# Optimization experiments

Measured on AMD Instinct MI355X. Metric: run time of the kernel, lower is better.

The kernel has to match this reference:

```python
import jax, jax.numpy as jnp
import numpy as np

N, E, F_IN, H, D = 50000, 800000, 128, 4, 32
NEG_SLOPE = 0.2

def setup_inputs() -> dict:
    key = jax.random.key(0)
    ks = jax.random.split(key, 8)
    x = jax.random.normal(ks[0], (N, F_IN), dtype=jnp.float32)
    src = jax.random.randint(ks[1], (E,), 0, N, dtype=jnp.int32)
    dst = jax.random.randint(ks[2], (E,), 0, N, dtype=jnp.int32)
    s = 1.0 / np.sqrt(F_IN)
    W_src = jax.random.uniform(ks[3], (F_IN, H * D), jnp.float32, -s, s)
    b_src = jnp.zeros((H * D,), jnp.float32)
    W_dst = jax.random.uniform(ks[4], (F_IN, H * D), jnp.float32, -s, s)
    b_dst = jnp.zeros((H * D,), jnp.float32)
    attn = jax.random.normal(ks[5], (H, D), dtype=jnp.float32) / np.sqrt(D)
    return {"x": x, "src": src, "dst": dst, "W_src": W_src, "b_src": b_src,
            "W_dst": W_dst, "b_dst": b_dst, "attn": attn}

def reference(x, src, dst, W_src, b_src, W_dst, b_dst, attn):
    n = x.shape[0]
    # dense projections: [N, H, D]
    fs = (x @ W_src + b_src).reshape(n, H, D)
    fd = (x @ W_dst + b_dst).reshape(n, H, D)
    # GATv2 edge score: a^T leaky_relu(W_l x_u + W_r x_v)
    e = jax.nn.leaky_relu(fs[src] + fd[dst], NEG_SLOPE)  # [E, H, D]
    score = jnp.einsum('ehd,hd->eh', e, attn)            # [E, H]
    # segment softmax over incoming edges of each dst node
    smax = jax.ops.segment_max(score, dst, num_segments=n)
    smax = jnp.where(jnp.isfinite(smax), smax, 0.0)
    ex = jnp.exp(score - smax[dst])
    denom = jax.ops.segment_sum(ex, dst, num_segments=n)
    alpha = ex / denom[dst]                              # [E, H]
    # scatter-weighted aggregation of src features
    h = jax.ops.segment_sum(alpha[:, :, None] * fs[src], dst, num_segments=n)
    h = jax.nn.relu(h)                                   # activation=relu
    return h.reshape(n, H * D)
```

## Files before the change

kernel.cpp:

```cpp
#include <hip/hip_runtime.h>
#include <hip/hip_fp16.h>

#define NN 50000
#define NE 800000
#define FIN 128
#define NH 4
#define HD 32
#define FOUT 128
#define NEG 0.2f
#define NB_W    ((256 * FIN + 255) / 256)
#define N_GEMM  782
#define NBKT    98
#define CHUNK   4096
#define NCHUNK  ((NE + CHUNK - 1) / CHUNK)
#define GB_GRID 980
#define BCAP    12288

typedef __attribute__((ext_vector_type(8))) short bf16x8;
typedef __attribute__((ext_vector_type(4))) float f32x4;

__device__ __forceinline__ uint f2bf_u(float f) {
    uint u = __float_as_uint(f);
    u += 0x7FFF + ((u >> 16) & 1);
    return u >> 16;
}
__device__ __forceinline__ ushort f2bf(float f) { return (ushort)f2bf_u(f); }

template<int CTRL>
__device__ __forceinline__ float dpp_add(float x) {
    int y = __builtin_amdgcn_update_dpp(0, __float_as_int(x), CTRL, 0xF, 0xF, false);
    return x + __int_as_float(y);
}
#define DPP_QUAD_XOR1 0xB1
#define DPP_QUAD_XOR2 0x4E

__device__ __forceinline__ __half2 u2h(uint u) { return __builtin_bit_cast(__half2, u); }
__device__ __forceinline__ uint h2u(__half2 h) { return __builtin_bit_cast(uint, h); }

__device__ __forceinline__ __half2 hmax2(__half2 a, __half2 b) {
    uint r, ua = h2u(a), ub = h2u(b);
    asm("v_pk_max_f16 %0, %1, %2" : "=v"(r) : "v"(ua), "v"(ub));
    return u2h(r);
}

__global__ __launch_bounds__(256) void hist_wt_k(
    const int* __restrict__ dst, int* __restrict__ chunk_hist,
    const float* __restrict__ Wsrc, const float* __restrict__ Wdst,
    ushort* __restrict__ Wt,
    const float* __restrict__ attn, __half* __restrict__ attn_h)
{
    __shared__ int hist[NBKT];
    const int b = blockIdx.x;
    const int tid = threadIdx.x;
    if (b < NCHUNK) {
        const int e0 = b * CHUNK;
        for (int t = tid; t < NBKT; t += 256) hist[t] = 0;
        __syncthreads();
        #pragma unroll
        for (int k = 0; k < 16; ++k) {
            const int e = e0 + k * 256 + tid;
            if (e < NE) atomicAdd(&hist[dst[e] >> 9], 1);
        }
        __syncthreads();
        for (int t = tid; t < NBKT; t += 256)
            chunk_hist[b * NBKT + t] = hist[t];
    } else {
        if (b == NCHUNK && tid < FOUT) attn_h[tid] = __float2half(attn[tid]);
        int t = (b - NCHUNK) * 256 + tid;
        if (t >= 256 * FIN) return;
        int n = t >> 7, k = t & 127;
        float v = (n < 128) ? Wsrc[k * 128 + n] : Wdst[k * 128 + (n - 128)];
        Wt[t] = f2bf(v);
    }
}

__global__ __launch_bounds__(256) void gemm_scatter_k(
    const float* __restrict__ x, const ushort* __restrict__ Wt,
    const float* __restrict__ bsrc, const float* __restrict__ bdst,
    __half* __restrict__ fsfd,
    const int* __restrict__ dst, const int* __restrict__ src,
    const int* __restrict__ chunk_hist, int* __restrict__ bkbase,
    uint* __restrict__ ebuf)
{
    __shared__ ushort As[64 * 128];
    __shared__ ushort Bs[64 * 128];
    __shared__ int cur[NBKT];
    __shared__ int tot_s[NBKT];
    __shared__ int par_s[NBKT];
    __shared__ int ps[256];
    const int b = blockIdx.x;
    const int tid = threadIdx.x;

    if (b % 5 == 0) {
        const int chunk = b / 5;
        for (int t = tid; t < NBKT; t += 256) { tot_s[t] = 0; par_s[t] = 0; }
        __syncthreads();
        #pragma unroll 4
        for (int i = tid; i < NCHUNK * NBKT; i += 256) {
            const int v = chunk_hist[i];
            const int c = i / NBKT;
            const int t = i - c * NBKT;
            atomicAdd(&tot_s[t], v);
            if (c < chunk) atomicAdd(&par_s[t], v);
        }
        __syncthreads();
        const int total = (tid < NBKT) ? tot_s[tid] : 0;
        ps[tid] = total;
        __syncthreads();
        for (int off = 1; off < 256; off <<= 1) {
            int add = (tid >= off) ? ps[tid - off] : 0;
            __syncthreads();
            ps[tid] += add;
            __syncthreads();
        }
        if (tid < NBKT) cur[tid] = (ps[tid] - total) + par_s[tid];
        if (chunk == 0) {
            if (tid < NBKT) bkbase[tid] = ps[tid] - total;
            if (tid == 0) bkbase[NBKT] = NE;
        }
        __syncthreads();
        const int e0 = chunk * CHUNK;
        #pragma unroll
        for (int k = 0; k < 16; ++k) {
            const int e = e0 + k * 256 + tid;
            if (e < NE) {
                const int d = dst[e];
                const int p = atomicAdd(&cur[d >> 9], 1);
                ebuf[p] = ((uint)d << 16) | (uint)src[e];
            }
        }
        return;
    }

    const int g = b - b / 5 - 1;
    if (g >= N_GEMM) return;
    const int bm = g * 64;

    for (int q = tid; q < 64 * 16; q += 256) {
        int r = q >> 4, c16 = q & 15;
        int row = bm + r;
        uint4 o = make_uint4(0u, 0u, 0u, 0u);
        if (row < NN) {
            const float4 a = *(const float4*)&x[(size_t)row * FIN + c16 * 8];
            const float4 c = *(const float4*)&x[(size_t)row * FIN + c16 * 8 + 4];
            o.x = f2bf_u(a.x) | (f2bf_u(a.y) << 16);
            o.y = f2bf_u(a.z) | (f2bf_u(a.w) << 16);
            o.z = f2bf_u(c.x) | (f2bf_u(c.y) << 16);
            o.w = f2bf_u(c.z) | (f2bf_u(c.w) << 16);
        }
        int off = r * 256 + ((c16 * 16) ^ ((r & 7) << 4));
        *(uint4*)((char*)As + off) = o;
    }

    const int wid = tid >> 6, lane = tid & 63;
    const int wr = (wid >> 1) * 32, wc = (wid & 1) * 32;
    const int lrow = lane & 15;
    const int lk = (lane >> 4) * 16;

    #pragma unroll
    for (int ct = 0; ct < 4; ++ct) {
        if (ct > 0) __syncthreads();
        for (int q = tid; q < 64 * 16; q += 256) {
            int r = q >> 4, c16 = q & 15;
            uint4 v = *(const uint4*)&Wt[(ct * 64 + r) * FIN + c16 * 8];
            int off = r * 256 + ((c16 * 16) ^ ((r & 7) << 4));
            *(uint4*)((char*)Bs + off) = v;
        }
        __syncthreads();

        f32x4 acc[2][2] = {};
        #pragma unroll
        for (int kk = 0; kk < 4; ++kk) {
            bf16x8 a[2], bb[2];
            #pragma unroll
            for (int m = 0; m < 2; ++m) {
                int r = wr + m * 16 + lrow;
                int off = r * 256 + ((kk * 64 + lk) ^ ((r & 7) << 4));
                a[m] = *(bf16x8*)((char*)As + off);
            }
            #pragma unroll
            for (int n = 0; n < 2; ++n) {
                int r = wc + n * 16 + lrow;
                int off = r * 256 + ((kk * 64 + lk) ^ ((r & 7) << 4));
                bb[n] = *(bf16x8*)((char*)Bs + off);
            }
            #pragma unroll
            for (int m = 0; m < 2; ++m)
                #pragma unroll
                for (int n = 0; n < 2; ++n)
                    acc[m][n] = __builtin_amdgcn_mfma_f32_16x16x32_bf16(a[m], bb[n], acc[m][n], 0, 0, 0);
        }

        #pragma unroll
        for (int m = 0; m < 2; ++m) {
            #pragma unroll
            for (int n = 0; n < 2; ++n) {
                int gcol = ct * 64 + wc + n * 16 + (lane & 15);
                float bias = (gcol < 128) ? bsrc[gcol] : bdst[gcol - 128];
                #pragma unroll
                for (int r = 0; r < 4; ++r) {
                    int grow = bm + wr + m * 16 + (lane >> 4) * 4 + r;
                    if (grow < NN)
                        fsfd[(size_t)grow * 256 + gcol] = __float2half(acc[m][n][r] + bias);
                }
            }
        }
    }
}

__global__ __launch_bounds__(256) void binB_k(
    const uint* __restrict__ ebuf, const int* __restrict__ bkbase,
    int* __restrict__ rowptr, ushort* __restrict__ nbr)
{
    __shared__ int cnt_s[512];
    __shared__ int ps[256];
    __shared__ ushort buf[BCAP];
    const int b = blockIdx.x;
    const int tid = threadIdx.x;
    const int node0 = b << 9;
    const int nodes = (node0 + 512 < NN) ? 512 : (NN - node0);
    const int segbase = bkbase[b];
    const int segend  = bkbase[b + 1];
    const int seglen  = segend - segbase;

    cnt_s[tid] = 0;
    cnt_s[tid + 256] = 0;
    __syncthreads();
    for (int i = segbase + tid; i < segend; i += 256)
        atomicAdd(&cnt_s[(int)(ebuf[i] >> 16) - node0], 1);
    __syncthreads();

    const int c0 = cnt_s[2 * tid], c1 = cnt_s[2 * tid + 1];
    const int pair = c0 + c1;
    ps[tid] = pair;
    __syncthreads();
    for (int off = 1; off < 256; off <<= 1) {
        int add = (tid >= off) ? ps[tid - off] : 0;
        __syncthreads();
        ps[tid] += add;
        __syncthreads();
    }
    const int ex = ps[tid] - pair;
    __syncthreads();
    cnt_s[2 * tid] = ex;
    cnt_s[2 * tid + 1] = ex + c0;
    if (2 * tid < nodes)     rowptr[node0 + 2 * tid]     = segbase + ex;
    if (2 * tid + 1 < nodes) rowptr[node0 + 2 * tid + 1] = segbase + ex + c0;
    if (b == NBKT - 1 && tid == 0) rowptr[NN] = segend;
    __syncthreads();

    if (seglen <= BCAP) {
        for (int i = segbase + tid; i < segend; i += 256) {
            const uint e = ebuf[i];
            const int d = (int)(e >> 16) - node0;
            const int p = atomicAdd(&cnt_s[d], 1);
            buf[p] = (ushort)(e & 0xffffu);
        }
        __syncthreads();
        for (int i = tid; i < seglen; i += 256)
            nbr[segbase + i] = buf[i];
    } else {
        for (int i = segbase + tid; i < segend; i += 256) {
            const uint e = ebuf[i];
            const int d = (int)(e >> 16) - node0;
            const int p = atomicAdd(&cnt_s[d], 1);
            nbr[segbase + p] = (ushort)(e & 0xffffu);
        }
    }
}

__global__ __launch_bounds__(256) void gat_node_k(
    const __half* __restrict__ fsfd, const __half* __restrict__ attn_h,
    const int* __restrict__ rowptr, const ushort* __restrict__ nbr,
    float* __restrict__ out)
{
    const int node = blockIdx.x * 4 + (threadIdx.x >> 6);
    const int lane = threadIdx.x & 63;
    const int ql = lane & 15;
    const int q  = lane >> 4;

    const uint4 ufd = *(const uint4*)&fsfd[(size_t)node * 256 + 128 + 8 * ql];
    const __half2 fd0 = u2h(ufd.x), fd1 = u2h(ufd.y), fd2 = u2h(ufd.z), fd3 = u2h(ufd.w);
    const uint4 uav = *(const uint4*)&attn_h[8 * ql];
    const __half2 av0 = u2h(uav.x), av1 = u2h(uav.y), av2 = u2h(uav.z), av3 = u2h(uav.w);
    const __half2 k02 = __float2half2_rn(NEG);

    const int beg = rowptr[node];
    const int end = rowptr[node + 1];

    float den = 0.f;
    __half2 acc0 = u2h(0), acc1 = u2h(0), acc2 = u2h(0), acc3 = u2h(0);

    for (int i = beg; i < end; i += 16) {
        #pragma unroll
        for (int j = 0; j < 4; ++j) {
            const int idx = i + 4 * j + q;
            const bool valid = idx < end;
            const int s = nbr[valid ? idx : end - 1];
            const uint4 u = *(const uint4*)&fsfd[(size_t)s * 256 + 8 * ql];
            const __half2 f0 = u2h(u.x), f1 = u2h(u.y), f2 = u2h(u.z), f3 = u2h(u.w);
            __half2 v0 = __hadd2(f0, fd0), v1 = __hadd2(f1, fd1);
            __half2 v2 = __hadd2(f2, fd2), v3 = __hadd2(f3, fd3);
            v0 = hmax2(v0, __hmul2(v0, k02));
            v1 = hmax2(v1, __hmul2(v1, k02));
            v2 = hmax2(v2, __hmul2(v2, k02));
            v3 = hmax2(v3, __hmul2(v3, k02));
            __half2 sch = __hmul2(v0, av0);
            sch = __hfma2(v1, av1, sch);
            sch = __hfma2(v2, av2, sch);
            sch = __hfma2(v3, av3, sch);
            float sc = __low2float(sch) + __high2float(sch);
            sc = dpp_add<DPP_QUAD_XOR1>(sc);
            sc = dpp_add<DPP_QUAD_XOR2>(sc);
            float ex = __expf(sc);
            ex = valid ? ex : 0.f;
            den += ex;
            const __half2 exh = __float2half2_rn(ex);
            acc0 = __hfma2(exh, f0, acc0);
            acc1 = __hfma2(exh, f1, acc1);
            acc2 = __hfma2(exh, f2, acc2);
            acc3 = __hfma2(exh, f3, acc3);
        }
    }

    den += __shfl_xor(den, 16, 64);
    den += __shfl_xor(den, 32, 64);
    uint ua0 = h2u(acc0), ua1 = h2u(acc1), ua2 = h2u(acc2), ua3 = h2u(acc3);
    ua0 = h2u(__hadd2(u2h(ua0), u2h((uint)__shfl_xor((int)ua0, 16, 64))));
    ua1 = h2u(__hadd2(u2h(ua1), u2h((uint)__shfl_xor((int)ua1, 16, 64))));
    ua2 = h2u(__hadd2(u2h(ua2), u2h((uint)__shfl_xor((int)ua2, 16, 64))));
    ua3 = h2u(__hadd2(u2h(ua3), u2h((uint)__shfl_xor((int)ua3, 16, 64))));
    ua0 = h2u(__hadd2(u2h(ua0), u2h((uint)__shfl_xor((int)ua0, 32, 64))));
    ua1 = h2u(__hadd2(u2h(ua1), u2h((uint)__shfl_xor((int)ua1, 32, 64))));
    ua2 = h2u(__hadd2(u2h(ua2), u2h((uint)__shfl_xor((int)ua2, 32, 64))));
    ua3 = h2u(__hadd2(u2h(ua3), u2h((uint)__shfl_xor((int)ua3, 32, 64))));

    if (q == 0) {
        const float inv = (den > 0.f) ? 1.f / den : 0.f;
        float4 o0, o1;
        o0.x = fmaxf(__low2float(u2h(ua0))  * inv, 0.f);
        o0.y = fmaxf(__high2float(u2h(ua0)) * inv, 0.f);
        o0.z = fmaxf(__low2float(u2h(ua1))  * inv, 0.f);
        o0.w = fmaxf(__high2float(u2h(ua1)) * inv, 0.f);
        o1.x = fmaxf(__low2float(u2h(ua2))  * inv, 0.f);
        o1.y = fmaxf(__high2float(u2h(ua2)) * inv, 0.f);
        o1.z = fmaxf(__low2float(u2h(ua3))  * inv, 0.f);
        o1.w = fmaxf(__high2float(u2h(ua3)) * inv, 0.f);
        *(float4*)&out[(size_t)node * FOUT + 8 * ql] = o0;
        *(float4*)&out[(size_t)node * FOUT + 8 * ql + 4] = o1;
    }
}

extern "C" void kernel_launch(void* const* d_in, const int* in_sizes, int n_in,
                              void* d_out, int out_size, void* d_ws, size_t ws_size,
                              hipStream_t stream)
{
    const float* x    = (const float*)d_in[0];
    const int*   src  = (const int*)d_in[1];
    const int*   dst  = (const int*)d_in[2];
    const float* Wsrc = (const float*)d_in[3];
    const float* bsrc = (const float*)d_in[4];
    const float* Wdst = (const float*)d_in[5];
    const float* bdst = (const float*)d_in[6];
    const float* attn = (const float*)d_in[7];
    float* out = (float*)d_out;

    ushort* Wt      = (ushort*)d_ws;
    __half* fsfd    = (__half*)(Wt + 256 * FIN);
    int* chunk_hist = (int*)(fsfd + (size_t)NN * 256);
    int* bkbase     = chunk_hist + NCHUNK * NBKT;
    int* rowptr     = bkbase + NBKT + 1;
    uint* ebuf      = (uint*)(rowptr + NN + 1);
    ushort* nbr     = (ushort*)(ebuf + NE);
    __half* attn_h  = (__half*)(nbr + NE);

    hist_wt_k<<<NCHUNK + NB_W, 256, 0, stream>>>(dst, chunk_hist, Wsrc, Wdst, Wt, attn, attn_h);
    gemm_scatter_k<<<GB_GRID, 256, 0, stream>>>(x, Wt, bsrc, bdst, fsfd,
                                                dst, src, chunk_hist, bkbase, ebuf);
    binB_k<<<NBKT, 256, 0, stream>>>(ebuf, bkbase, rowptr, nbr);
    gat_node_k<<<(NN + 3) / 4, 256, 0, stream>>>(fsfd, attn_h, rowptr, nbr, out);
}
```

Measured before the change: 92.10 us.

## Split fused GEMM/scatter kernel and transpose MFMA operands for vectorized stores

Splits the combined GEMM and edge-scatter kernel into two separate kernels. The scatter kernel no longer carries the GEMM's 32KB shared memory, so it can run at higher occupancy, and the GEMM is launched after binning. The MFMA operands are swapped so each lane holds four consecutive output columns, which lets the epilogue write packed 8-byte half stores with a float4 bias load instead of scalar stores. It also adds an extra kernel launch and gives up the overlap between GEMM and scatter work.

```diff
diff --git a/kernel.cpp b/kernel.cpp
--- a/kernel.cpp
+++ b/kernel.cpp
@@ -13,7 +13,6 @@
 #define NBKT    98
 #define CHUNK   4096
 #define NCHUNK  ((NE + CHUNK - 1) / CHUNK)
-#define GB_GRID 980
 #define BCAP    12288
 
 typedef __attribute__((ext_vector_type(8))) short bf16x8;
@@ -25,6 +24,9 @@
     return u >> 16;
 }
 __device__ __forceinline__ ushort f2bf(float f) { return (ushort)f2bf_u(f); }
+__device__ __forceinline__ uint f2h_u(float f) {
+    return (uint)__builtin_bit_cast(ushort, __float2half(f));
+}
 
 template<int CTRL>
 __device__ __forceinline__ float dpp_add(float x) {
@@ -74,67 +76,65 @@
     }
 }
 
-__global__ __launch_bounds__(256) void gemm_scatter_k(
-    const float* __restrict__ x, const ushort* __restrict__ Wt,
-    const float* __restrict__ bsrc, const float* __restrict__ bdst,
-    __half* __restrict__ fsfd,
+__global__ __launch_bounds__(256) void scatter_k(
     const int* __restrict__ dst, const int* __restrict__ src,
     const int* __restrict__ chunk_hist, int* __restrict__ bkbase,
     uint* __restrict__ ebuf)
 {
-    __shared__ ushort As[64 * 128];
-    __shared__ ushort Bs[64 * 128];
     __shared__ int cur[NBKT];
     __shared__ int tot_s[NBKT];
     __shared__ int par_s[NBKT];
     __shared__ int ps[256];
-    const int b = blockIdx.x;
+    const int chunk = blockIdx.x;
     const int tid = threadIdx.x;
 
-    if (b % 5 == 0) {
-        const int chunk = b / 5;
-        for (int t = tid; t < NBKT; t += 256) { tot_s[t] = 0; par_s[t] = 0; }
-        __syncthreads();
-        #pragma unroll 4
-        for (int i = tid; i < NCHUNK * NBKT; i += 256) {
-            const int v = chunk_hist[i];
-            const int c = i / NBKT;
-            const int t = i - c * NBKT;
-            atomicAdd(&tot_s[t], v);
-            if (c < chunk) atomicAdd(&par_s[t], v);
-        }
-        __syncthreads();
-        const int total = (tid < NBKT) ? tot_s[tid] : 0;
-        ps[tid] = total;
-        __syncthreads();
-        for (int off = 1; off < 256; off <<= 1) {
-            int add = (tid >= off) ? ps[tid - off] : 0;
-            __syncthreads();
-            ps[tid] += add;
-            __syncthreads();
-        }
-        if (tid < NBKT) cur[tid] = (ps[tid] - total) + par_s[tid];
-        if (chunk == 0) {
-            if (tid < NBKT) bkbase[tid] = ps[tid] - total;
-            if (tid == 0) bkbase[NBKT] = NE;
-        }
-        __syncthreads();
-        const int e0 = chunk * CHUNK;
-        #pragma unroll
-        for (int k = 0; k < 16; ++k) {
-            const int e = e0 + k * 256 + tid;
-            if (e < NE) {
-                const int d = dst[e];
-                const int p = atomicAdd(&cur[d >> 9], 1);
-                ebuf[p] = ((uint)d << 16) | (uint)src[e];
-            }
-        }
-        return;
-    }
-
-    const int g = b - b / 5 - 1;
-    if (g >= N_GEMM) return;
-    const int bm = g * 64;
+    for (int t = tid; t < NBKT; t += 256) { tot_s[t] = 0; par_s[t] = 0; }
+    __syncthreads();
+    #pragma unroll 4
+    for (int i = tid; i < NCHUNK * NBKT; i += 256) {
+        const int v = chunk_hist[i];
+        const int c = i / NBKT;
+        const int t = i - c * NBKT;
+        atomicAdd(&tot_s[t], v);
+        if (c < chunk) atomicAdd(&par_s[t], v);
+    }
+    __syncthreads();
+    const int total = (tid < NBKT) ? tot_s[tid] : 0;
+    ps[tid] = total;
+    __syncthreads();
+    for (int off = 1; off < 256; off <<= 1) {
+        int add = (tid >= off) ? ps[tid - off] : 0;
+        __syncthreads();
+        ps[tid] += add;
+        __syncthreads();
+    }
+    if (tid < NBKT) cur[tid] = (ps[tid] - total) + par_s[tid];
+    if (chunk == 0) {
+        if (tid < NBKT) bkbase[tid] = ps[tid] - total;
+        if (tid == 0) bkbase[NBKT] = NE;
+    }
+    __syncthreads();
+    const int e0 = chunk * CHUNK;
+    #pragma unroll
+    for (int k = 0; k < 16; ++k) {
+        const int e = e0 + k * 256 + tid;
+        if (e < NE) {
+            const int d = dst[e];
+            const int p = atomicAdd(&cur[d >> 9], 1);
+            ebuf[p] = ((uint)d << 16) | (uint)src[e];
+        }
+    }
+}
+
+__global__ __launch_bounds__(256) void gemm_k(
+    const float* __restrict__ x, const ushort* __restrict__ Wt,
+    const float* __restrict__ bsrc, const float* __restrict__ bdst,
+    __half* __restrict__ fsfd)
+{
+    __shared__ ushort As[64 * 128];
+    __shared__ ushort Bs[64 * 128];
+    const int tid = threadIdx.x;
+    const int bm = blockIdx.x * 64;
 
     for (int q = tid; q < 64 * 16; q += 256) {
         int r = q >> 4, c16 = q & 15;
@@ -188,21 +188,21 @@
             for (int m = 0; m < 2; ++m)
                 #pragma unroll
                 for (int n = 0; n < 2; ++n)
-                    acc[m][n] = __builtin_amdgcn_mfma_f32_16x16x32_bf16(a[m], bb[n], acc[m][n], 0, 0, 0);
+                    acc[m][n] = __builtin_amdgcn_mfma_f32_16x16x32_bf16(bb[n], a[m], acc[m][n], 0, 0, 0);
         }
 
         #pragma unroll
         for (int m = 0; m < 2; ++m) {
+            const int grow = bm + wr + m * 16 + (lane & 15);
+            if (grow >= NN) continue;
             #pragma unroll
             for (int n = 0; n < 2; ++n) {
-                int gcol = ct * 64 + wc + n * 16 + (lane & 15);
-                float bias = (gcol < 128) ? bsrc[gcol] : bdst[gcol - 128];
-                #pragma unroll
-                for (int r = 0; r < 4; ++r) {
-                    int grow = bm + wr + m * 16 + (lane >> 4) * 4 + r;
-                    if (grow < NN)
-                        fsfd[(size_t)grow * 256 + gcol] = __float2half(acc[m][n][r] + bias);
-                }
+                const int gcolb = ct * 64 + wc + n * 16 + (lane >> 4) * 4;
+                const float4 b4 = (gcolb < 128) ? *(const float4*)&bsrc[gcolb]
+                                                : *(const float4*)&bdst[gcolb - 128];
+                uint lo = f2h_u(acc[m][n][0] + b4.x) | (f2h_u(acc[m][n][1] + b4.y) << 16);
+                uint hi = f2h_u(acc[m][n][2] + b4.z) | (f2h_u(acc[m][n][3] + b4.w) << 16);
+                *(uint2*)&fsfd[(size_t)grow * 256 + gcolb] = make_uint2(lo, hi);
             }
         }
     }
@@ -375,8 +375,8 @@
     __half* attn_h  = (__half*)(nbr + NE);
 
     hist_wt_k<<<NCHUNK + NB_W, 256, 0, stream>>>(dst, chunk_hist, Wsrc, Wdst, Wt, attn, attn_h);
-    gemm_scatter_k<<<GB_GRID, 256, 0, stream>>>(x, Wt, bsrc, bdst, fsfd,
-                                                dst, src, chunk_hist, bkbase, ebuf);
+    scatter_k<<<NCHUNK, 256, 0, stream>>>(dst, src, chunk_hist, bkbase, ebuf);
     binB_k<<<NBKT, 256, 0, stream>>>(ebuf, bkbase, rowptr, nbr);
+    gemm_k<<<N_GEMM, 256, 0, stream>>>(x, Wt, bsrc, bdst, fsfd);
     gat_node_k<<<(NN + 3) / 4, 256, 0, stream>>>(fsfd, attn_h, rowptr, nbr, out);
 }
```

Measured after the change: 107.5 us. 1.17x slower.
